# Performance work log

Hardware: AMD Instinct MI355X
Metric: run time of the kernel (lower is better)

## Reference

```python
import jax, jax.numpy as jnp
import numpy as np

B, NQ, NK, D, H = 4, 1025, 1024, 1024, 16
C = D // H          # per-head channels = 64
DFF = 1024          # FFN hidden, hard-coded in source
LN_EPS = 1e-5


def setup_inputs() -> dict:
    key = jax.random.key(0)
    ks = jax.random.split(key, 12)
    s = 0.02
    return {
        "q": jax.random.normal(ks[0], (B, NQ, D), jnp.float32),
        "k": jax.random.normal(ks[1], (B, NK, D), jnp.float32),
        "v": jax.random.normal(ks[2], (B, NK, D), jnp.float32),
        "w_qk": jax.random.normal(ks[3], (D, D), jnp.float32) * s,
        "dummy": jax.random.normal(ks[4], (1, D), jnp.float32),
        "w1": jax.random.normal(ks[5], (C, C // 2), jnp.float32) * s,
        "b1": jnp.zeros((C // 2,), jnp.float32),
        "w2": jax.random.normal(ks[6], (C, C // 2), jnp.float32) * s,
        "b2": jnp.zeros((C // 2,), jnp.float32),
        "w3": jax.random.normal(ks[7], (2 * C, C), jnp.float32) * s,
        "b3": jnp.zeros((C,), jnp.float32),
        "fw1": jax.random.normal(ks[8], (C, DFF), jnp.float32) * s,
        "fb1": jnp.zeros((DFF,), jnp.float32),
        "fw2": jax.random.normal(ks[9], (DFF, C), jnp.float32) * s,
        "fb2": jnp.zeros((C,), jnp.float32),
        "ln_g": jnp.ones((C,), jnp.float32),
        "ln_b": jnp.zeros((C,), jnp.float32),
    }


def _split_heads(x):
    # 'b n (h c) -> (b h) n c'
    b, n, _ = x.shape
    return x.reshape(b, n, H, C).transpose(0, 2, 1, 3).reshape(b * H, n, C)


def _l2norm(x):
    n = jnp.linalg.norm(x, axis=-1, keepdims=True)
    return x / jnp.maximum(n, 1e-12)


def reference(q, k, v, w_qk, dummy, w1, b1, w2, b2, w3, b3,
              fw1, fb1, fw2, fb2, ln_g, ln_b):
    b, nq, d = q.shape
    residual = q
    qp = q @ w_qk
    kp = jnp.concatenate(
        [k @ w_qk, jnp.broadcast_to(dummy[None], (b, 1, d))], axis=1)
    vp = jnp.concatenate([v, jnp.zeros((b, 1, d), v.dtype)], axis=1)

    qh, kh, vh, rh = map(_split_heads, (qp, kp, vp, residual))

    # cosine-similarity attention, ReLU instead of softmax (dropout p=0)
    attn = jnp.einsum('bic,bjc->bij', _l2norm(qh), _l2norm(kh))
    attn = jax.nn.relu(attn)
    out = jnp.einsum('bij,bjc->bic', attn, vh)  # (b*h, nq, c)

    o1 = jax.nn.relu((out * rh) @ w1 + b1)
    o2 = jax.nn.relu((rh - out) @ w2 + b2)
    o = jnp.concatenate([o1, o2, rh], axis=-1) @ w3 + b3

    # FFN with residual + LayerNorm (dropouts are identity at p=0)
    t = o + rh
    t = t + (jax.nn.relu(t @ fw1 + fb1) @ fw2 + fb2)
    mu = jnp.mean(t, axis=-1, keepdims=True)
    var = jnp.mean(jnp.square(t - mu), axis=-1, keepdims=True)
    t = (t - mu) / jnp.sqrt(var + LN_EPS) * ln_g + ln_b

    t = t + vh  # requires nq == nk + 1

    # '(b h) n c -> b n (h c)'
    return t.reshape(b, H, nq, C).transpose(0, 2, 1, 3).reshape(b, nq, d)
```

## Files before the change

### kernel.cpp

```cpp
#include <hip/hip_runtime.h>
#include <hip/hip_bf16.h>

#define DEV __device__ __forceinline__

typedef __attribute__((ext_vector_type(4))) float  f32x4;
typedef __attribute__((ext_vector_type(8))) short  s16x8;
typedef __attribute__((ext_vector_type(8))) __bf16 bf16x8;

#define NQ   1025
#define BH   64
#define NPAD 1152
#define MT   65600
#define DFF  1024

DEV short f2bf(float f){
  unsigned u = __builtin_bit_cast(unsigned, f);
  u = u + 0x7fffu + ((u >> 16) & 1u);
  return (short)(u >> 16);
}
DEV float bf2f(short s){
  unsigned u = ((unsigned)(unsigned short)s) << 16;
  return __builtin_bit_cast(float, u);
}
DEV f32x4 zero4(){ f32x4 z; z[0]=0.f; z[1]=0.f; z[2]=0.f; z[3]=0.f; return z; }
DEV s16x8 zero8(){ s16x8 z; for(int e=0;e<8;e++) z[e]=0; return z; }

DEV f32x4 mfma16(s16x8 a, s16x8 b, f32x4 c){
  return __builtin_amdgcn_mfma_f32_16x16x32_bf16(
      __builtin_bit_cast(bf16x8, a), __builtin_bit_cast(bf16x8, b), c, 0, 0, 0);
}

DEV void gll16(const void* g, void* l){
  __builtin_amdgcn_global_load_lds((const __attribute__((address_space(1))) void*)g,
                                   (__attribute__((address_space(3))) void*)l, 16, 0, 0);
}

DEV s16x8 lds_frag(const char* base, int row, int k8){
  int byte = row*128 + k8*2; byte ^= (row & 7) << 4;
  return *(const s16x8*)(base + byte);
}
DEV void lds_write16(char* base, int row, int k8, s16x8 v){
  int byte = row*128 + k8*2; byte ^= (row & 7) << 4;
  *(s16x8*)(base + byte) = v;
}
DEV void lds_write2(char* base, int row, int col, short v){
  int byte = row*128 + col*2; byte ^= (row & 7) << 4;
  *(short*)(base + byte) = v;
}
DEV void lds_w16_256(char* base, int row, int col, s16x8 v){
  int byte = row*256 + col*2; byte ^= (row & 7) << 4;
  *(s16x8*)(base + byte) = v;
}
DEV s16x8 lds_r16_256(const char* base, int row, int col){
  int byte = row*256 + col*2; byte ^= (row & 7) << 4;
  return *(const s16x8*)(base + byte);
}
DEV void lds_w2_256(char* base, int row, int col, short v){
  int byte = row*256 + col*2; byte ^= (row & 7) << 4;
  *(short*)(base + byte) = v;
}
DEV void blob_w16(char* blob, int row, int k8, s16x8 v){
  int byte = row*128 + k8*2; byte ^= (row & 7) << 4;
  *(s16x8*)(blob + byte) = v;
}

__global__ __launch_bounds__(256)
void k_cvtA(const float* __restrict__ q, const float* __restrict__ kk, char* __restrict__ ab){
  int mt = blockIdx.x, kt = blockIdx.y;
  int tid = threadIdx.x;
  int r = tid>>1, ks = (tid&1)*32;
  int pr = mt*128 + r;
  int part = pr >= 4608;
  int pp = part ? pr-4608 : pr;
  int b = pp/NPAD, i = pp%NPAD;
  const float* src = nullptr;
  if (!part && i < 1025) src = q  + ((long)(b*1025+i))*1024 + kt*64 + ks;
  if ( part && i < 1024) src = kk + ((long)(b*1024+i))*1024 + kt*64 + ks;
  char* blob = ab + ((long)(mt*16+kt))*16384;
  #pragma unroll
  for (int c8=0;c8<32;c8+=8){
    s16x8 vv = zero8();
    if (src){
      f32x4 f0 = *(const f32x4*)(src + c8);
      f32x4 f1 = *(const f32x4*)(src + c8 + 4);
      #pragma unroll
      for(int e=0;e<4;e++){ vv[e]=f2bf(f0[e]); vv[4+e]=f2bf(f1[e]); }
    }
    blob_w16(blob, r, ks+c8, vv);
  }
}

__global__ __launch_bounds__(256)
void k_cvtW(const float* __restrict__ w, char* __restrict__ wb){
  __shared__ float T[64][129];
  int nt = blockIdx.x, kt = blockIdx.y;
  int tid = threadIdx.x;
  for (int idx=tid; idx<8192; idx+=256){
    int kr = idx>>7, nc = idx&127;
    T[kr][nc] = w[(long)(kt*64+kr)*1024 + nt*128+nc];
  }
  __syncthreads();
  int r = tid>>1, ks=(tid&1)*32;
  char* blob = wb + ((long)(nt*16+kt))*16384;
  #pragma unroll
  for (int c8=0;c8<32;c8+=8){
    s16x8 vv;
    #pragma unroll
    for(int e=0;e<8;e++) vv[e] = f2bf(T[ks+c8+e][r]);
    blob_w16(blob, r, ks+c8, vv);
  }
}

__global__ __launch_bounds__(256)
void k_cvtV(const float* __restrict__ v, char* __restrict__ vb){
  __shared__ float T[64][65];
  int jt = blockIdx.x, bh = blockIdx.y;
  int b = bh>>4, h = bh&15;
  int tid=threadIdx.x;
  for (int idx=tid; idx<4096; idx+=256){
    int jr = idx>>6, cc = idx&63;
    int j = jt*64+jr;
    T[jr][cc] = (j<1024)? v[((long)(b*1024+j))*1024 + h*64+cc] : 0.f;
  }
  __syncthreads();
  int r = tid>>2, js=(tid&3)*16;
  char* blob = vb + ((long)(bh*18+jt))*8192;
  #pragma unroll
  for (int c8=0;c8<16;c8+=8){
    s16x8 vv;
    #pragma unroll
    for(int e=0;e<8;e++) vv[e] = f2bf(T[js+c8+e][r]);
    blob_w16(blob, r, js+c8, vv);
  }
}

__global__ __launch_bounds__(256)
void k_cvtFB(const float* __restrict__ fw1, const float* __restrict__ fw2,
             char* __restrict__ f1B, char* __restrict__ f2B){
  __shared__ float T[64][65];
  int d = blockIdx.x, which = blockIdx.y;
  int tid = threadIdx.x;
  for (int idx=tid; idx<4096; idx+=256){
    int r = idx>>6, c = idx&63;
    T[r][c] = (which==0) ? fw1[(long)r*DFF + d*64 + c]
                         : fw2[(long)(d*64+r)*64 + c];
  }
  __syncthreads();
  char* blob = (which==0 ? f1B : f2B) + (long)d*8192;
  int rr = tid>>2, js = (tid&3)*16;
  #pragma unroll
  for (int c8=0;c8<16;c8+=8){
    s16x8 vv;
    #pragma unroll
    for(int e=0;e<8;e++) vv[e] = f2bf(T[js+c8+e][rr]);
    blob_w16(blob, rr, js+c8, vv);
  }
}

__global__ __launch_bounds__(256,2)
void k_proj(const char* __restrict__ ab, const char* __restrict__ wb,
            char* __restrict__ qpB, char* __restrict__ kpB,
            float* __restrict__ qnorm, float* __restrict__ knorm){
  __shared__ char SM[32768];
  char* A = SM; char* Bm = SM+16384;
  int flat = blockIdx.x;
  int g = (flat&7)*72 + (flat>>3);
  int mt = g>>3, nt = g&7;
  int tid=threadIdx.x, lane=tid&63, wv=tid>>6, lr=lane&15, lg=lane>>4;
  f32x4 acc[4][4];
  for(int a=0;a<4;a++) for(int b=0;b<4;b++) acc[a][b]=zero4();
  int wm=(wv>>1)*64, wn=(wv&1)*64;
  for (int kt=0; kt<16; kt++){
    const char* asrc = ab + ((long)(mt*16+kt))*16384 + wv*4096 + lane*16;
    const char* bsrc = wb + ((long)(nt*16+kt))*16384 + wv*4096 + lane*16;
    char* adst = A + wv*4096;  char* bdst = Bm + wv*4096;
    #pragma unroll
    for (int t=0;t<4;t++){
      gll16(asrc + t*1024, adst + t*1024);
      gll16(bsrc + t*1024, bdst + t*1024);
    }
    __syncthreads();
    #pragma unroll
    for (int kc=0;kc<64;kc+=32){
      int lk = kc + (lg<<3);
      s16x8 af[4], bfr[4];
      #pragma unroll
      for(int i=0;i<4;i++) af[i]  = lds_frag(A,  wm + i*16 + lr, lk);
      #pragma unroll
      for(int i=0;i<4;i++) bfr[i] = lds_frag(Bm, wn + i*16 + lr, lk);
      #pragma unroll
      for(int mi=0;mi<4;mi++)
        #pragma unroll
        for(int ni=0;ni<4;ni++) acc[mi][ni] = mfma16(af[mi], bfr[ni], acc[mi][ni]);
    }
    __syncthreads();
  }
  int head = nt*2 + (wv&1);
  #pragma unroll
  for(int mi=0;mi<4;mi++)
  #pragma unroll
  for(int j=0;j<4;j++){
    float ss = 0.f;
    #pragma unroll
    for(int ni=0;ni<4;ni++){ float x=acc[mi][ni][j]; ss += x*x; }
    ss += __shfl_xor(ss,1); ss += __shfl_xor(ss,2);
    ss += __shfl_xor(ss,4); ss += __shfl_xor(ss,8);
    if (lr==0){
      int pr = mt*128 + wm + mi*16 + lg*4 + j;
      int part = pr>=4608; int pp = part? pr-4608:pr;
      int b = pp/NPAD, i = pp%NPAD;
      float scv = 1.f/fmaxf(sqrtf(ss), 1e-12f);
      (part? knorm : qnorm)[(b*16+head)*NPAD + i] = scv;
    }
  }
  #pragma unroll
  for(int mi=0;mi<4;mi++)
  #pragma unroll
  for(int ni=0;ni<4;ni++)
  #pragma unroll
  for(int j=0;j<4;j++)
    lds_w2_256(SM, wm+mi*16+lg*4+j, wn+ni*16+lr, f2bf(acc[mi][ni][j]));
  __syncthreads();
  {
    int r = tid>>1, half = tid&1;
    int pr = mt*128 + r;
    int part = pr>=4608; int pp = part? pr-4608:pr;
    int b = pp/NPAD, i = pp%NPAD;
    int h2 = nt*2 + half;
    char* dst = (part? kpB : qpB) + ((long)((b*16+h2)*18 + (i>>6)))*8192;
    int rr = i&63;
    #pragma unroll
    for (int c8=0;c8<64;c8+=8){
      s16x8 vv = lds_r16_256(SM, r, half*64 + c8);
      blob_w16(dst, rr, c8, vv);
    }
  }
}

__global__ __launch_bounds__(256,2)
void k_attn(const char* __restrict__ qpB, const char* __restrict__ kpB,
            const char* __restrict__ vtB,
            const float* __restrict__ qnorm, const float* __restrict__ knorm,
            short* __restrict__ att){
  __shared__ char SM[49152];
  char* Q = SM; char* KT = SM+16384; char* VT = KT+8192; char* P = VT+8192;
  int flat = blockIdx.x;
  int g = (flat&7)*72 + (flat>>3);
  int bh = g/9, it = g%9;
  int i0 = it*128;
  int tid=threadIdx.x, lane=tid&63, wv=tid>>6, lr=lane&15, lg=lane>>4;
  {
    const char* src = qpB + ((long)(bh*18 + it*2))*8192 + wv*4096 + lane*16;
    char* dst = Q + wv*4096;
    #pragma unroll
    for (int t=0;t<4;t++) gll16(src + t*1024, dst + t*1024);
  }
  float rq[2][4];
  #pragma unroll
  for(int mi=0;mi<2;mi++)
  #pragma unroll
  for(int j=0;j<4;j++)
    rq[mi][j] = qnorm[bh*NPAD + i0 + wv*32+mi*16+lg*4+j];
  f32x4 oacc[2][4];
  for(int a=0;a<2;a++) for(int b=0;b<4;b++) oacc[a][b]=zero4();
  for (int jt=0; jt<18; ++jt){
    {
      const char* ks = kpB + ((long)(bh*18+jt))*8192 + wv*2048 + lane*16;
      const char* vs = vtB + ((long)(bh*18+jt))*8192 + wv*2048 + lane*16;
      gll16(ks,      KT + wv*2048);
      gll16(ks+1024, KT + wv*2048 + 1024);
      gll16(vs,      VT + wv*2048);
      gll16(vs+1024, VT + wv*2048 + 1024);
    }
    float rk[4];
    #pragma unroll
    for(int ni=0;ni<4;ni++) rk[ni] = knorm[bh*NPAD + jt*64 + ni*16+lr];
    __syncthreads();
    f32x4 sc[2][4];
    for(int a=0;a<2;a++) for(int b=0;b<4;b++) sc[a][b]=zero4();
    #pragma unroll
    for(int kc=0;kc<64;kc+=32){
      int lk = kc + (lg<<3);
      s16x8 af[2], bfr[4];
      #pragma unroll
      for(int i=0;i<2;i++) af[i]=lds_frag(Q, wv*32 + i*16 + lr, lk);
      #pragma unroll
      for(int i=0;i<4;i++) bfr[i]=lds_frag(KT, i*16 + lr, lk);
      #pragma unroll
      for(int mi=0;mi<2;mi++)
        #pragma unroll
        for(int ni=0;ni<4;ni++) sc[mi][ni]=mfma16(af[mi],bfr[ni],sc[mi][ni]);
    }
    #pragma unroll
    for(int mi=0;mi<2;mi++)
    #pragma unroll
    for(int ni=0;ni<4;ni++)
    #pragma unroll
    for(int j=0;j<4;j++){
      float x = sc[mi][ni][j] * rq[mi][j] * rk[ni];
      x = x>0.f?x:0.f;
      lds_write2(P, wv*32 + mi*16 + lg*4 + j, ni*16 + lr, f2bf(x));
    }
    __syncthreads();
    #pragma unroll
    for(int kc=0;kc<64;kc+=32){
      int lk = kc + (lg<<3);
      s16x8 pf[2], vf[4];
      #pragma unroll
      for(int i=0;i<2;i++) pf[i]=lds_frag(P, wv*32 + i*16 + lr, lk);
      #pragma unroll
      for(int i=0;i<4;i++) vf[i]=lds_frag(VT, i*16 + lr, lk);
      #pragma unroll
      for(int mi=0;mi<2;mi++)
        #pragma unroll
        for(int ni=0;ni<4;ni++) oacc[mi][ni]=mfma16(pf[mi],vf[ni],oacc[mi][ni]);
    }
    __syncthreads();
  }
  char* OS = SM+16384;
  #pragma unroll
  for(int mi=0;mi<2;mi++)
  #pragma unroll
  for(int ni=0;ni<4;ni++)
  #pragma unroll
  for(int j=0;j<4;j++)
    lds_write2(OS, wv*32+mi*16+lg*4+j, ni*16+lr, f2bf(oacc[mi][ni][j]));
  __syncthreads();
  {
    int r = tid>>1, half = tid&1;
    int i = i0 + r;
    if (i < 1025){
      short* dst = att + ((long)bh*1025 + i)*64 + half*32;
      #pragma unroll
      for (int u=0; u<32; u+=8){
        s16x8 vv = lds_frag(OS, r, half*32 + u);
        *(s16x8*)(dst + u) = vv;
      }
    }
  }
}

__global__ __launch_bounds__(512,4)
void k_tailpre(const short* __restrict__ att, const float* __restrict__ q,
    const float* __restrict__ w1, const float* __restrict__ b1,
    const float* __restrict__ w2, const float* __restrict__ b2,
    const float* __restrict__ w3, const float* __restrict__ b3,
    float* __restrict__ tf){
  __shared__ char SM[73728];
  char* R1 = SM;
  char* R2 = SM + 16384;
  char* R3 = SM + 32768;
  char* WA = SM + 49152;
  char* WB = SM + 53248;
  char* W3 = SM + 57344;
  long m0 = (long)blockIdx.x*128;
  int tid=threadIdx.x, lane=tid&63, wv=tid>>6, lr=lane&15, lg=lane>>4;
  int wr0 = wv*16;
  for (int idx=tid; idx<2048; idx+=512){
    int n=idx>>6, c=idx&63;
    lds_write2(WA, n, c, f2bf(w1[c*32+n]));
    lds_write2(WB, n, c, f2bf(w2[c*32+n]));
  }
  for (int idx=tid; idx<8192; idx+=512){
    int n=idx>>7, kx=idx&127;
    lds_w2_256(W3, n, kx, f2bf(w3[kx*64+n]));
  }
  {
    int r = tid>>2, ks=(tid&3)*16;
    long m = m0 + r;
    if (m < MT){
      int bh=(int)(m/1025); int i=(int)(m-(long)bh*1025); int b=bh>>4, h=bh&15;
      const short* asrc = att + m*64 + ks;
      const float* qsrc = q + ((long)b*1025+i)*1024 + h*64 + ks;
      #pragma unroll
      for (int c8=0;c8<16;c8+=8){
        s16x8 av = *(const s16x8*)(asrc + c8);
        f32x4 q0 = *(const f32x4*)(qsrc + c8);
        f32x4 q1 = *(const f32x4*)(qsrc + c8 + 4);
        s16x8 x1v,x2v,rhv;
        #pragma unroll
        for(int e=0;e<4;e++){
          float o0=bf2f(av[e]),   r0=q0[e];
          float o1=bf2f(av[4+e]), r1=q1[e];
          x1v[e]=f2bf(o0*r0);   x1v[4+e]=f2bf(o1*r1);
          x2v[e]=f2bf(r0-o0);   x2v[4+e]=f2bf(r1-o1);
          rhv[e]=f2bf(r0);      rhv[4+e]=f2bf(r1);
        }
        lds_write16(R1, r, ks+c8, x1v);
        lds_write16(R2, r, ks+c8, x2v);
        lds_write16(R3, r, ks+c8, rhv);
      }
    } else {
      s16x8 z = zero8();
      #pragma unroll
      for (int c8=0;c8<16;c8+=8){
        lds_write16(R1, r, ks+c8, z);
        lds_write16(R2, r, ks+c8, z);
        lds_write16(R3, r, ks+c8, z);
      }
    }
  }
  __syncthreads();
  f32x4 a1[4];
  #pragma unroll
  for(int ni=0;ni<4;ni++) a1[ni]=zero4();
  #pragma unroll
  for (int kc=0;kc<64;kc+=32){
    int lk = kc + (lg<<3);
    s16x8 af1 = lds_frag(R1, wr0+lr, lk);
    s16x8 af2 = lds_frag(R2, wr0+lr, lk);
    s16x8 bw1[2], bw2[2];
    #pragma unroll
    for(int i=0;i<2;i++){
      bw1[i]=lds_frag(WA, i*16+lr, lk);
      bw2[i]=lds_frag(WB, i*16+lr, lk);
    }
    #pragma unroll
    for(int ni=0;ni<2;ni++){
      a1[ni]   = mfma16(af1, bw1[ni], a1[ni]);
      a1[2+ni] = mfma16(af2, bw2[ni], a1[2+ni]);
    }
  }
  float bias12[4];
  #pragma unroll
  for(int ni=0;ni<4;ni++){ int cc=ni*16+lr; bias12[ni] = (cc<32)? b1[cc] : b2[cc-32]; }
  #pragma unroll
  for(int ni=0;ni<4;ni++)
  #pragma unroll
  for(int j=0;j<4;j++){
    float x = a1[ni][j] + bias12[ni];
    x = x>0.f?x:0.f;
    lds_write2(R1, wr0+lg*4+j, ni*16+lr, f2bf(x));
  }
  f32x4 a2[4];
  #pragma unroll
  for(int ni=0;ni<4;ni++) a2[ni]=zero4();
  #pragma unroll
  for (int kc=0;kc<64;kc+=32){
    int lk = kc + (lg<<3);
    s16x8 ao = lds_frag(R1, wr0+lr, lk);
    s16x8 ar = lds_frag(R3, wr0+lr, lk);
    s16x8 bo[4], br[4];
    #pragma unroll
    for(int i=0;i<4;i++){
      bo[i]=lds_r16_256(W3, i*16+lr, lk);
      br[i]=lds_r16_256(W3, i*16+lr, 64+lk);
    }
    #pragma unroll
    for(int ni=0;ni<4;ni++){
      a2[ni]=mfma16(ao, bo[ni], a2[ni]);
      a2[ni]=mfma16(ar, br[ni], a2[ni]);
    }
  }
  float b3v[4];
  #pragma unroll
  for(int ni=0;ni<4;ni++) b3v[ni] = b3[ni*16+lr];
  #pragma unroll
  for(int j=0;j<4;j++){
    long m = m0 + wr0 + lg*4 + j;
    if (m < MT){
      int bh=(int)(m/1025); int i=(int)(m-(long)bh*1025); int b=bh>>4, h=bh&15;
      const float* qsrc = q + ((long)b*1025+i)*1024 + h*64;
      #pragma unroll
      for(int ni=0;ni<4;ni++){
        int cc = ni*16+lr;
        tf[m*64+cc] = a2[ni][j] + b3v[ni] + qsrc[cc];
      }
    }
  }
}

__global__ __launch_bounds__(256,3)
void k_ffn(const float* __restrict__ tf,
      const char* __restrict__ f1B, const char* __restrict__ f2B,
      const float* __restrict__ fb1, const float* __restrict__ fb2,
      const float* __restrict__ ln_g, const float* __restrict__ ln_b,
      const float* __restrict__ v, float* __restrict__ out){
  __shared__ char SM[49152];
  char* T  = SM;
  char* U  = SM + 16384;
  char* W1 = SM + 32768;
  char* W2 = SM + 40960;
  long m0 = (long)blockIdx.x*128;
  int tid=threadIdx.x, lane=tid&63, wv=tid>>6, lr=lane&15, lg=lane>>4;
  {
    int r=tid>>1, ks=(tid&1)*32; long m=m0+r;
    #pragma unroll
    for(int c8=0;c8<32;c8+=8){
      s16x8 vv = zero8();
      if (m<MT){
        f32x4 f0 = *(const f32x4*)(tf + m*64 + ks + c8);
        f32x4 f1 = *(const f32x4*)(tf + m*64 + ks + c8 + 4);
        #pragma unroll
        for(int e=0;e<4;e++){ vv[e]=f2bf(f0[e]); vv[4+e]=f2bf(f1[e]); }
      }
      lds_write16(T, r, ks+c8, vv);
    }
  }
  f32x4 acc2[2][4];
  for(int a=0;a<2;a++) for(int b=0;b<4;b++) acc2[a][b]=zero4();
  for (int d=0; d<16; ++d){
    {
      const char* s1 = f1B + (long)d*8192 + wv*2048 + lane*16;
      const char* s2 = f2B + (long)d*8192 + wv*2048 + lane*16;
      gll16(s1,        W1 + wv*2048);
      gll16(s1 + 1024, W1 + wv*2048 + 1024);
      gll16(s2,        W2 + wv*2048);
      gll16(s2 + 1024, W2 + wv*2048 + 1024);
    }
    __syncthreads();
    f32x4 sc[2][4];
    for(int a=0;a<2;a++) for(int b=0;b<4;b++) sc[a][b]=zero4();
    #pragma unroll
    for(int kc=0;kc<64;kc+=32){
      int lk = kc + (lg<<3);
      s16x8 af[2], bfr[4];
      #pragma unroll
      for(int i=0;i<2;i++) af[i]=lds_frag(T, wv*32+i*16+lr, lk);
      #pragma unroll
      for(int i=0;i<4;i++) bfr[i]=lds_frag(W1, i*16+lr, lk);
      #pragma unroll
      for(int mi=0;mi<2;mi++)
        #pragma unroll
        for(int ni=0;ni<4;ni++) sc[mi][ni]=mfma16(af[mi],bfr[ni],sc[mi][ni]);
    }
    #pragma unroll
    for(int mi=0;mi<2;mi++)
    #pragma unroll
    for(int ni=0;ni<4;ni++)
    #pragma unroll
    for(int j=0;j<4;j++){
      int uc = ni*16+lr;
      float x = sc[mi][ni][j] + fb1[d*64+uc];
      x = x>0.f?x:0.f;
      lds_write2(U, wv*32+mi*16+lg*4+j, uc, f2bf(x));
    }
    #pragma unroll
    for(int kc=0;kc<64;kc+=32){
      int lk = kc + (lg<<3);
      s16x8 uf[2], wf[4];
      #pragma unroll
      for(int i=0;i<2;i++) uf[i]=lds_frag(U, wv*32+i*16+lr, lk);
      #pragma unroll
      for(int i=0;i<4;i++) wf[i]=lds_frag(W2, i*16+lr, lk);
      #pragma unroll
      for(int mi=0;mi<2;mi++)
        #pragma unroll
        for(int ni=0;ni<4;ni++) acc2[mi][ni]=mfma16(uf[mi],wf[ni],acc2[mi][ni]);
    }
    __syncthreads();
  }
  #pragma unroll
  for(int mi=0;mi<2;mi++){
    float xv[4][4];
    long mbase = m0 + wv*32 + mi*16 + lg*4;
    #pragma unroll
    for(int ni=0;ni<4;ni++)
    #pragma unroll
    for(int j=0;j<4;j++){
      long m = mbase + j;
      int c = ni*16+lr;
      float t = (m<MT)? tf[m*64+c] : 0.f;
      xv[ni][j] = acc2[mi][ni][j] + fb2[c] + t;
    }
    #pragma unroll
    for(int j=0;j<4;j++){
      float s = xv[0][j]+xv[1][j]+xv[2][j]+xv[3][j];
      #pragma unroll
      for(int mm=1;mm<16;mm<<=1) s += __shfl_xor(s, mm);
      float mu = s*(1.f/64.f);
      float vs = 0.f;
      #pragma unroll
      for(int ni=0;ni<4;ni++){ float d2=xv[ni][j]-mu; vs += d2*d2; }
      #pragma unroll
      for(int mm=1;mm<16;mm<<=1) vs += __shfl_xor(vs, mm);
      float inv = rsqrtf(vs*(1.f/64.f) + 1e-5f);
      long m = mbase + j;
      if (m < MT){
        int bh = (int)(m/1025); int i = (int)(m - (long)bh*1025);
        int b = bh>>4, h = bh&15;
        #pragma unroll
        for(int ni=0;ni<4;ni++){
          int c = ni*16+lr;
          float y = (xv[ni][j]-mu)*inv*ln_g[c] + ln_b[c];
          float vh = (i<1024)? v[((long)b*1024 + i)*1024 + h*64 + c] : 0.f;
          out[((long)b*1025 + i)*1024 + h*64 + c] = y + vh;
        }
      }
    }
  }
}

extern "C" void kernel_launch(void* const* d_in, const int* in_sizes, int n_in,
                              void* d_out, int out_size, void* d_ws, size_t ws_size,
                              hipStream_t stream) {
  const float* q    = (const float*)d_in[0];
  const float* k    = (const float*)d_in[1];
  const float* v    = (const float*)d_in[2];
  const float* w_qk = (const float*)d_in[3];
  const float* w1   = (const float*)d_in[5];
  const float* b1   = (const float*)d_in[6];
  const float* w2   = (const float*)d_in[7];
  const float* b2   = (const float*)d_in[8];
  const float* w3   = (const float*)d_in[9];
  const float* b3   = (const float*)d_in[10];
  const float* fw1  = (const float*)d_in[11];
  const float* fb1  = (const float*)d_in[12];
  const float* fw2  = (const float*)d_in[13];
  const float* fb2  = (const float*)d_in[14];
  const float* ln_g = (const float*)d_in[15];
  const float* ln_b = (const float*)d_in[16];
  float* out = (float*)d_out;

  char* ws = (char*)d_ws;
  const size_t OFF_A   = 0;
  const size_t SZ_A    = 25190400;
  const size_t OFF_WB  = OFF_A + SZ_A;
  const size_t OFF_F1B = OFF_WB  + (size_t)8*16*16384;
  const size_t OFF_F2B = OFF_F1B + (size_t)16*8192;
  const size_t OFF_VT  = OFF_F2B + (size_t)16*8192;
  const size_t OFF_QP  = OFF_VT  + (size_t)64*18*8192;
  const size_t OFF_KP  = OFF_QP  + (size_t)64*18*8192;
  const size_t OFF_QN  = OFF_KP  + (size_t)64*18*8192;
  const size_t OFF_KN  = OFF_QN  + (size_t)BH*NPAD*4;
  const size_t NEEDED  = OFF_KN  + (size_t)BH*NPAD*4;
  if (ws_size < NEEDED) return;

  char*  ab   = ws + OFF_A;
  short* att  = (short*)(ws + OFF_A);
  float* tf   = (float*)(ws + OFF_A + 8396800);
  char*  wb   = ws + OFF_WB;
  char*  f1B  = ws + OFF_F1B;
  char*  f2B  = ws + OFF_F2B;
  char*  vtB  = ws + OFF_VT;
  char*  qpB  = ws + OFF_QP;
  char*  kpB  = ws + OFF_KP;
  float* qnorm= (float*)(ws + OFF_QN);
  float* knorm= (float*)(ws + OFF_KN);

  k_cvtA<<<dim3(72,16), 256, 0, stream>>>(q, k, ab);
  k_cvtW<<<dim3(8,16),  256, 0, stream>>>(w_qk, wb);
  k_cvtV<<<dim3(18,64), 256, 0, stream>>>(v, vtB);
  k_cvtFB<<<dim3(16,2), 256, 0, stream>>>(fw1, fw2, f1B, f2B);
  k_proj<<<576, 256, 0, stream>>>(ab, wb, qpB, kpB, qnorm, knorm);
  k_attn<<<576, 256, 0, stream>>>(qpB, kpB, vtB, qnorm, knorm, att);
  k_tailpre<<<513, 512, 0, stream>>>(att, q, w1, b1, w2, b2, w3, b3, tf);
  k_ffn<<<513, 256, 0, stream>>>(tf, f1B, f2B, fb1, fb2, ln_g, ln_b, v, out);
}
```

Measured before the change: 193.3 us.

## Double-buffer K/V tiles in attention and weight tiles in FFN kernel

```diff
diff --git a/kernel.cpp b/kernel.cpp
--- a/kernel.cpp
+++ b/kernel.cpp
@@ -242,8 +242,11 @@
             const char* __restrict__ vtB,
             const float* __restrict__ qnorm, const float* __restrict__ knorm,
             short* __restrict__ att){
-  __shared__ char SM[49152];
-  char* Q = SM; char* KT = SM+16384; char* VT = KT+8192; char* P = VT+8192;
+  __shared__ char SM[65536];
+  char* Q   = SM;
+  char* P   = SM + 16384;
+  char* KTb = SM + 32768;
+  char* VTb = SM + 49152;
   int flat = blockIdx.x;
   int g = (flat&7)*72 + (flat>>3);
   int bh = g/9, it = g%9;
@@ -255,6 +258,14 @@
     #pragma unroll
     for (int t=0;t<4;t++) gll16(src + t*1024, dst + t*1024);
   }
+  {
+    const char* ks = kpB + ((long)(bh*18))*8192 + wv*2048 + lane*16;
+    const char* vs = vtB + ((long)(bh*18))*8192 + wv*2048 + lane*16;
+    gll16(ks,      KTb + wv*2048);
+    gll16(ks+1024, KTb + wv*2048 + 1024);
+    gll16(vs,      VTb + wv*2048);
+    gll16(vs+1024, VTb + wv*2048 + 1024);
+  }
   float rq[2][4];
   #pragma unroll
   for(int mi=0;mi<2;mi++)
@@ -263,19 +274,23 @@
     rq[mi][j] = qnorm[bh*NPAD + i0 + wv*32+mi*16+lg*4+j];
   f32x4 oacc[2][4];
   for(int a=0;a<2;a++) for(int b=0;b<4;b++) oacc[a][b]=zero4();
+  __syncthreads();
+  int p = 0;
   for (int jt=0; jt<18; ++jt){
-    {
-      const char* ks = kpB + ((long)(bh*18+jt))*8192 + wv*2048 + lane*16;
-      const char* vs = vtB + ((long)(bh*18+jt))*8192 + wv*2048 + lane*16;
-      gll16(ks,      KT + wv*2048);
-      gll16(ks+1024, KT + wv*2048 + 1024);
-      gll16(vs,      VT + wv*2048);
-      gll16(vs+1024, VT + wv*2048 + 1024);
-    }
+    if (jt < 17){
+      int pn = p^1;
+      const char* ks = kpB + ((long)(bh*18+jt+1))*8192 + wv*2048 + lane*16;
+      const char* vs = vtB + ((long)(bh*18+jt+1))*8192 + wv*2048 + lane*16;
+      gll16(ks,      KTb + pn*8192 + wv*2048);
+      gll16(ks+1024, KTb + pn*8192 + wv*2048 + 1024);
+      gll16(vs,      VTb + pn*8192 + wv*2048);
+      gll16(vs+1024, VTb + pn*8192 + wv*2048 + 1024);
+    }
+    const char* KT = KTb + p*8192;
+    const char* VT = VTb + p*8192;
     float rk[4];
     #pragma unroll
     for(int ni=0;ni<4;ni++) rk[ni] = knorm[bh*NPAD + jt*64 + ni*16+lr];
-    __syncthreads();
     f32x4 sc[2][4];
     for(int a=0;a<2;a++) for(int b=0;b<4;b++) sc[a][b]=zero4();
     #pragma unroll
@@ -301,7 +316,6 @@
       x = x>0.f?x:0.f;
       lds_write2(P, wv*32 + mi*16 + lg*4 + j, ni*16 + lr, f2bf(x));
     }
-    __syncthreads();
     #pragma unroll
     for(int kc=0;kc<64;kc+=32){
       int lk = kc + (lg<<3);
@@ -316,8 +330,9 @@
         for(int ni=0;ni<4;ni++) oacc[mi][ni]=mfma16(pf[mi],vf[ni],oacc[mi][ni]);
     }
     __syncthreads();
-  }
-  char* OS = SM+16384;
+    p ^= 1;
+  }
+  char* OS = KTb;
   #pragma unroll
   for(int mi=0;mi<2;mi++)
   #pragma unroll
@@ -470,17 +485,17 @@
   }
 }
 
-__global__ __launch_bounds__(256,3)
+__global__ __launch_bounds__(256,2)
 void k_ffn(const float* __restrict__ tf,
       const char* __restrict__ f1B, const char* __restrict__ f2B,
       const float* __restrict__ fb1, const float* __restrict__ fb2,
       const float* __restrict__ ln_g, const float* __restrict__ ln_b,
       const float* __restrict__ v, float* __restrict__ out){
-  __shared__ char SM[49152];
-  char* T  = SM;
-  char* U  = SM + 16384;
-  char* W1 = SM + 32768;
-  char* W2 = SM + 40960;
+  __shared__ char SM[65536];
+  char* T   = SM;
+  char* U   = SM + 16384;
+  char* W1b = SM + 32768;
+  char* W2b = SM + 49152;
   long m0 = (long)blockIdx.x*128;
   int tid=threadIdx.x, lane=tid&63, wv=tid>>6, lr=lane&15, lg=lane>>4;
   {
@@ -497,18 +512,30 @@
       lds_write16(T, r, ks+c8, vv);
     }
   }
+  {
+    const char* s1 = f1B + wv*2048 + lane*16;
+    const char* s2 = f2B + wv*2048 + lane*16;
+    gll16(s1,        W1b + wv*2048);
+    gll16(s1 + 1024, W1b + wv*2048 + 1024);
+    gll16(s2,        W2b + wv*2048);
+    gll16(s2 + 1024, W2b + wv*2048 + 1024);
+  }
   f32x4 acc2[2][4];
   for(int a=0;a<2;a++) for(int b=0;b<4;b++) acc2[a][b]=zero4();
+  __syncthreads();
+  int p = 0;
   for (int d=0; d<16; ++d){
-    {
-      const char* s1 = f1B + (long)d*8192 + wv*2048 + lane*16;
-      const char* s2 = f2B + (long)d*8192 + wv*2048 + lane*16;
-      gll16(s1,        W1 + wv*2048);
-      gll16(s1 + 1024, W1 + wv*2048 + 1024);
-      gll16(s2,        W2 + wv*2048);
-      gll16(s2 + 1024, W2 + wv*2048 + 1024);
-    }
-    __syncthreads();
+    if (d < 15){
+      int pn = p^1;
+      const char* s1 = f1B + (long)(d+1)*8192 + wv*2048 + lane*16;
+      const char* s2 = f2B + (long)(d+1)*8192 + wv*2048 + lane*16;
+      gll16(s1,        W1b + pn*8192 + wv*2048);
+      gll16(s1 + 1024, W1b + pn*8192 + wv*2048 + 1024);
+      gll16(s2,        W2b + pn*8192 + wv*2048);
+      gll16(s2 + 1024, W2b + pn*8192 + wv*2048 + 1024);
+    }
+    const char* W1 = W1b + p*8192;
+    const char* W2 = W2b + p*8192;
     f32x4 sc[2][4];
     for(int a=0;a<2;a++) for(int b=0;b<4;b++) sc[a][b]=zero4();
     #pragma unroll
@@ -549,6 +576,7 @@
         for(int ni=0;ni<4;ni++) acc2[mi][ni]=mfma16(uf[mi],wf[ni],acc2[mi][ni]);
     }
     __syncthreads();
+    p ^= 1;
   }
   #pragma unroll
   for(int mi=0;mi<2;mi++){
```

After: 214.7 us. 1.11x slower.
